# Optimization experiments

Hardware: AMD Instinct MI355X
Metric: run time of the kernel (lower is better)

The kernel has to match this reference:

```python
import jax, jax.numpy as jnp
import numpy as np

TOPK = 4
TEMP = 1.0
BN_EPS = 1e-5


def setup_inputs() -> dict:
    key = jax.random.key(0)
    ks = jax.random.split(key, 5)
    B, H, W = 8, 256, 256
    return {
        "img": jax.random.uniform(ks[0], (B, 3, H, W), dtype=jnp.float32),
        "feat": jax.random.normal(ks[1], (B, 64, H, W), dtype=jnp.float32),
        "w_bneck": jax.random.normal(ks[2], (16, 64), dtype=jnp.float32) * 0.1,
        "b_bneck": jax.random.normal(ks[3], (16,), dtype=jnp.float32) * 0.1,
        "gamma": jnp.ones((16,), dtype=jnp.float32),
        "beta": jnp.zeros((16,), dtype=jnp.float32),
        "w_mask": jax.random.normal(ks[4], (256, 16), dtype=jnp.float32) * 0.1,
        "num_colors": 64,
    }


def reference(img, feat, w_bneck, b_bneck, gamma, beta, w_mask, num_colors):
    B, _, H, W = img.shape
    # bottleneck: 1x1 conv + BatchNorm (training stats) + ReLU
    x = jnp.einsum('bchw,oc->bohw', feat, w_bneck) + b_bneck[None, :, None, None]
    mu = x.mean(axis=(0, 2, 3))
    var = x.var(axis=(0, 2, 3))
    x = (x - mu[None, :, None, None]) * jax.lax.rsqrt(var + BN_EPS)[None, :, None, None]
    x = jax.nn.relu(x * gamma[None, :, None, None] + beta[None, :, None, None])
    # color_mask: bias-free 1x1 conv -> [B, 256, H, W]
    m = jnp.einsum('bchw,oc->bohw', x, w_mask)
    # agg == 'mean': [B, 256//num_colors, num_colors, H, W].mean(1)
    m = m.reshape(B, -1, num_colors, H, W).mean(axis=1)  # [B, nc, H, W]
    # per-pixel topk over color channel + softmax + scatter mask
    k = min(TOPK, num_colors)
    m_l = jnp.transpose(m, (0, 2, 3, 1))          # [B, H, W, nc]
    vals, idx = jax.lax.top_k(m_l, k)             # [B, H, W, k]
    sm = jax.nn.softmax(vals / TEMP, axis=-1)
    bi = jnp.arange(B)[:, None, None, None]
    hi = jnp.arange(H)[None, :, None, None]
    wi = jnp.arange(W)[None, None, :, None]
    m_scat = jnp.zeros_like(m_l).at[bi, hi, wi, idx].set(sm)
    m = jnp.transpose(m_scat, (0, 3, 1, 2))       # [B, nc, H, W]
    # weighted color palette: [B, 3, nc, 1, 1]
    num = jnp.einsum('bchw,bnhw->bcn', img, m)
    den = m.sum(axis=(2, 3))                      # [B, nc]
    color_palette = (num / (den[:, None, :] + 1e-8))[:, :, :, None, None]
    # train-mode reconstruction
    transformed_img = jnp.einsum('bnhw,bcn->bchw', m, color_palette[:, :, :, 0, 0])
    return (transformed_img, m, color_palette)
```

## Files before the change

kernel.cpp:

```cpp
#include <hip/hip_runtime.h>

typedef long long ll;

#define PPI   65536
#define NPIX  524288
#define NCH   64
#define NB    16
#define NC    64
#define BN_EPS 1e-5

__global__ __launch_bounds__(256) void k_conv(const float* __restrict__ feat,
                                              const float* __restrict__ wb,
                                              double* __restrict__ gsum,
                                              double* __restrict__ gsq,
                                              float* __restrict__ xout)
{
    const int tid = threadIdx.x;
    const int wave = tid >> 6, lane = tid & 63;
    const int b   = blockIdx.x >> 6;
    const int p0  = ((blockIdx.x & 63) << 10) + (tid << 2);
    const float* fb = feat + (ll)b * NCH * PPI + p0;

    float4 acc[NB];
#pragma unroll
    for (int o = 0; o < NB; ++o) acc[o] = make_float4(0.f, 0.f, 0.f, 0.f);

#pragma unroll 4
    for (int c = 0; c < NCH; ++c) {
        float4 f = *reinterpret_cast<const float4*>(fb + (ll)c * PPI);
#pragma unroll
        for (int o = 0; o < NB; ++o) {
            float wv = wb[o * NCH + c];
            acc[o].x = fmaf(f.x, wv, acc[o].x);
            acc[o].y = fmaf(f.y, wv, acc[o].y);
            acc[o].z = fmaf(f.z, wv, acc[o].z);
            acc[o].w = fmaf(f.w, wv, acc[o].w);
        }
    }

#pragma unroll
    for (int o = 0; o < NB; ++o)
        *reinterpret_cast<float4*>(xout + ((ll)(b * NC + 48 + o)) * PPI + p0) = acc[o];

    __shared__ float red_s[4][NB], red_q[4][NB];
#pragma unroll
    for (int o = 0; o < NB; ++o) {
        float s = (acc[o].x + acc[o].y) + (acc[o].z + acc[o].w);
        float q = fmaf(acc[o].x, acc[o].x, acc[o].y * acc[o].y) +
                  fmaf(acc[o].z, acc[o].z, acc[o].w * acc[o].w);
#pragma unroll
        for (int off = 32; off > 0; off >>= 1) {
            s += __shfl_down(s, off);
            q += __shfl_down(q, off);
        }
        if (lane == 0) { red_s[wave][o] = s; red_q[wave][o] = q; }
    }
    __syncthreads();
    if (tid < NB) {
        atomicAdd(&gsum[tid], (double)red_s[0][tid] + red_s[1][tid] + red_s[2][tid] + red_s[3][tid]);
        atomicAdd(&gsq[tid],  (double)red_q[0][tid] + red_q[1][tid] + red_q[2][tid] + red_q[3][tid]);
    }
}

__global__ __launch_bounds__(256) void k_mask(const float* __restrict__ img,
                                              const float* __restrict__ gamma,
                                              const float* __restrict__ beta,
                                              const float* __restrict__ wm,
                                              const double* __restrict__ gsum,
                                              const double* __restrict__ gsq,
                                              float* __restrict__ den_g,
                                              float* __restrict__ num_g,
                                              float* m_out,
                                              unsigned* __restrict__ idx_out,
                                              float* __restrict__ sm_out)
{
    __shared__ float weff_l[NC][NB];
    __shared__ float den_loc[4][NC];
    __shared__ float num_loc[4][3 * NC];
    __shared__ float scl_l[NB], shf_l[NB];

    const int tid = threadIdx.x;
    const int wave = tid >> 6;
    const int b   = blockIdx.x >> 6;
    const int p0  = ((blockIdx.x & 63) << 10) + (tid << 2);

    for (int i = tid; i < NC * NB; i += 256) {
        int n = i >> 4, o = i & 15;
        weff_l[n][o] = 0.25f * (wm[n * NB + o] + wm[(64 + n) * NB + o] +
                                wm[(128 + n) * NB + o] + wm[(192 + n) * NB + o]);
    }
    for (int i = tid; i < 4 * NC; i += 256) den_loc[i >> 6][i & 63] = 0.f;
    for (int i = tid; i < 4 * 3 * NC; i += 256) num_loc[i / (3 * NC)][i % (3 * NC)] = 0.f;
    if (tid < NB) {
        double mu  = gsum[tid] * (1.0 / NPIX);
        double var = gsq[tid] * (1.0 / NPIX) - mu * mu;
        double sc  = (double)gamma[tid] / sqrt(var + BN_EPS);
        scl_l[tid] = (float)sc;
        shf_l[tid] = (float)((double)beta[tid] - mu * sc);
    }
    __syncthreads();

    float4 xx[NB];
#pragma unroll
    for (int o = 0; o < NB; ++o)
        xx[o] = *reinterpret_cast<const float4*>(m_out + ((ll)(b * NC + 48 + o)) * PPI + p0);
#pragma unroll
    for (int o = 0; o < NB; ++o) {
        float sc = scl_l[o], sh = shf_l[o];
        xx[o].x = fmaxf(0.f, fmaf(xx[o].x, sc, sh));
        xx[o].y = fmaxf(0.f, fmaf(xx[o].y, sc, sh));
        xx[o].z = fmaxf(0.f, fmaf(xx[o].z, sc, sh));
        xx[o].w = fmaxf(0.f, fmaf(xx[o].w, sc, sh));
    }

    float tv[4][4];
    int   ti[4][4];
#pragma unroll
    for (int j = 0; j < 4; ++j)
#pragma unroll
        for (int k = 0; k < 4; ++k) { tv[j][k] = -3.4e38f; ti[j][k] = 0; }

#pragma unroll 2
    for (int n = 0; n < NC; ++n) {
        const float* wr = weff_l[n];
        float4 v = make_float4(0.f, 0.f, 0.f, 0.f);
#pragma unroll
        for (int o = 0; o < NB; ++o) {
            float w = wr[o];
            v.x = fmaf(xx[o].x, w, v.x);
            v.y = fmaf(xx[o].y, w, v.y);
            v.z = fmaf(xx[o].z, w, v.z);
            v.w = fmaf(xx[o].w, w, v.w);
        }
        float vv[4] = {v.x, v.y, v.z, v.w};
#pragma unroll
        for (int j = 0; j < 4; ++j) {
            float x = vv[j];
            bool c0 = x > tv[j][0];
            bool c1 = x > tv[j][1];
            bool c2 = x > tv[j][2];
            bool c3 = x > tv[j][3];
            tv[j][3] = c2 ? tv[j][2] : fmaxf(x, tv[j][3]);
            ti[j][3] = c2 ? ti[j][2] : (c3 ? n : ti[j][3]);
            tv[j][2] = c1 ? tv[j][1] : fmaxf(x, tv[j][2]);
            ti[j][2] = c1 ? ti[j][1] : (c2 ? n : ti[j][2]);
            tv[j][1] = c0 ? tv[j][0] : fmaxf(x, tv[j][1]);
            ti[j][1] = c0 ? ti[j][0] : (c1 ? n : ti[j][1]);
            tv[j][0] = fmaxf(x, tv[j][0]);
            ti[j][0] = c0 ? n : ti[j][0];
        }
    }

    float smx[4][4];
#pragma unroll
    for (int j = 0; j < 4; ++j) {
        float e1 = expf(tv[j][1] - tv[j][0]);
        float e2 = expf(tv[j][2] - tv[j][0]);
        float e3 = expf(tv[j][3] - tv[j][0]);
        float rz = 1.f / (1.f + e1 + e2 + e3);
        smx[j][0] = rz; smx[j][1] = e1 * rz; smx[j][2] = e2 * rz; smx[j][3] = e3 * rz;
    }

#define SEL(j, n) (((ti[j][0] == (n)) ? smx[j][0] : 0.f) + \
                   ((ti[j][1] == (n)) ? smx[j][1] : 0.f) + \
                   ((ti[j][2] == (n)) ? smx[j][2] : 0.f) + \
                   ((ti[j][3] == (n)) ? smx[j][3] : 0.f))
#pragma unroll 1
    for (int n = 0; n < NC; ++n) {
        float4 mv;
        mv.x = SEL(0, n); mv.y = SEL(1, n); mv.z = SEL(2, n); mv.w = SEL(3, n);
        *reinterpret_cast<float4*>(m_out + ((ll)(b * NC + n)) * PPI + p0) = mv;
    }
#undef SEL

    ll gp = (ll)b * PPI + p0;
    uint4 pk;
    pk.x = (unsigned)ti[0][0] | ((unsigned)ti[0][1] << 8) | ((unsigned)ti[0][2] << 16) | ((unsigned)ti[0][3] << 24);
    pk.y = (unsigned)ti[1][0] | ((unsigned)ti[1][1] << 8) | ((unsigned)ti[1][2] << 16) | ((unsigned)ti[1][3] << 24);
    pk.z = (unsigned)ti[2][0] | ((unsigned)ti[2][1] << 8) | ((unsigned)ti[2][2] << 16) | ((unsigned)ti[2][3] << 24);
    pk.w = (unsigned)ti[3][0] | ((unsigned)ti[3][1] << 8) | ((unsigned)ti[3][2] << 16) | ((unsigned)ti[3][3] << 24);
    *reinterpret_cast<uint4*>(idx_out + gp) = pk;
#pragma unroll
    for (int k = 0; k < 4; ++k) {
        float4 sv = make_float4(smx[0][k], smx[1][k], smx[2][k], smx[3][k]);
        *reinterpret_cast<float4*>(sm_out + (ll)k * NPIX + gp) = sv;
    }

    float4 i0 = *reinterpret_cast<const float4*>(img + ((ll)b * 3 + 0) * PPI + p0);
    float4 i1 = *reinterpret_cast<const float4*>(img + ((ll)b * 3 + 1) * PPI + p0);
    float4 i2 = *reinterpret_cast<const float4*>(img + ((ll)b * 3 + 2) * PPI + p0);
    float ir0[4] = {i0.x, i0.y, i0.z, i0.w};
    float ir1[4] = {i1.x, i1.y, i1.z, i1.w};
    float ir2[4] = {i2.x, i2.y, i2.z, i2.w};
#pragma unroll
    for (int j = 0; j < 4; ++j) {
#pragma unroll
        for (int k = 0; k < 4; ++k) {
            float s = smx[j][k];
            int   n = ti[j][k];
            atomicAdd(&den_loc[wave][n], s);
            atomicAdd(&num_loc[wave][0 * NC + n], s * ir0[j]);
            atomicAdd(&num_loc[wave][1 * NC + n], s * ir1[j]);
            atomicAdd(&num_loc[wave][2 * NC + n], s * ir2[j]);
        }
    }
    __syncthreads();
    if (tid < NC)
        atomicAdd(&den_g[b * NC + tid],
                  den_loc[0][tid] + den_loc[1][tid] + den_loc[2][tid] + den_loc[3][tid]);
    if (tid < 3 * NC)
        atomicAdd(&num_g[(ll)b * 3 * NC + tid],
                  num_loc[0][tid] + num_loc[1][tid] + num_loc[2][tid] + num_loc[3][tid]);
}

__global__ __launch_bounds__(256) void k_recon(const unsigned* __restrict__ idx_in,
                                               const float* __restrict__ sm_in,
                                               const float* __restrict__ den_g,
                                               const float* __restrict__ num_g,
                                               float* __restrict__ pal_out,
                                               float* __restrict__ t_out)
{
    __shared__ float pal_l[3][NC];
    __shared__ float rden[NC];
    const int tid = threadIdx.x;
    const int b   = blockIdx.x >> 6;
    const int p0  = ((blockIdx.x & 63) << 10) + (tid << 2);

    if (tid < NC) rden[tid] = 1.f / (den_g[b * NC + tid] + 1e-8f);
    __syncthreads();
    if (tid < 3 * NC) {
        int c = tid >> 6, n = tid & 63;
        pal_l[c][n] = num_g[(ll)b * 3 * NC + tid] * rden[n];
    }
    __syncthreads();
    if ((blockIdx.x & 63) == 0 && tid < 3 * NC)
        pal_out[b * 3 * NC + tid] = pal_l[tid >> 6][tid & 63];

    ll gp = (ll)b * PPI + p0;
    uint4 pk  = *reinterpret_cast<const uint4*>(idx_in + gp);
    float4 s0 = *reinterpret_cast<const float4*>(sm_in + gp);
    float4 s1 = *reinterpret_cast<const float4*>(sm_in + (ll)NPIX + gp);
    float4 s2 = *reinterpret_cast<const float4*>(sm_in + 2ll * NPIX + gp);
    float4 s3 = *reinterpret_cast<const float4*>(sm_in + 3ll * NPIX + gp);
    unsigned pkv[4] = {pk.x, pk.y, pk.z, pk.w};
    float sA[4][4] = {{s0.x, s1.x, s2.x, s3.x}, {s0.y, s1.y, s2.y, s3.y},
                      {s0.z, s1.z, s2.z, s3.z}, {s0.w, s1.w, s2.w, s3.w}};

#pragma unroll
    for (int c = 0; c < 3; ++c) {
        float4 t;
        float* tp = &t.x;
#pragma unroll
        for (int j = 0; j < 4; ++j) {
            unsigned p = pkv[j];
            tp[j] = sA[j][0] * pal_l[c][p & 255] + sA[j][1] * pal_l[c][(p >> 8) & 255] +
                    sA[j][2] * pal_l[c][(p >> 16) & 255] + sA[j][3] * pal_l[c][p >> 24];
        }
        *reinterpret_cast<float4*>(t_out + ((ll)b * 3 + c) * PPI + p0) = t;
    }
}

extern "C" void kernel_launch(void* const* d_in, const int* in_sizes, int n_in,
                              void* d_out, int out_size, void* d_ws, size_t ws_size,
                              hipStream_t stream)
{
    const float* img   = (const float*)d_in[0];
    const float* feat  = (const float*)d_in[1];
    const float* wb    = (const float*)d_in[2];
    const float* gamma = (const float*)d_in[4];
    const float* beta  = (const float*)d_in[5];
    const float* wm    = (const float*)d_in[6];

    char* ws = (char*)d_ws;
    double*   gsum  = (double*)(ws + 0);
    double*   gsq   = (double*)(ws + 128);
    float*    den_g = (float*)(ws + 256);
    float*    num_g = (float*)(ws + 2304);
    unsigned* idx4  = (unsigned*)(ws + 8448);
    float*    smarr = (float*)(ws + 8448 + 4ll * NPIX);

    float* t_out   = (float*)d_out;
    float* m_out   = t_out + 3ll * NPIX;
    float* pal_out = m_out + 64ll * NPIX;

    hipMemsetAsync(ws, 0, 8448, stream);

    k_conv <<<NPIX / 1024, 256, 0, stream>>>(feat, wb, gsum, gsq, m_out);
    k_mask <<<NPIX / 1024, 256, 0, stream>>>(img, gamma, beta, wm, gsum, gsq,
                                             den_g, num_g, m_out, idx4, smarr);
    k_recon<<<NPIX / 1024, 256, 0, stream>>>(idx4, smarr, den_g, num_g, pal_out, t_out);
}
```

Before: 356.0 us.

## Process one pixel per thread and raise occupancy across all three kernels

Each thread now handles one pixel instead of four, and the grid is four times larger in all three kernels. Launch bounds now request 8 blocks per CU. The aim is to cut per-thread register pressure so more waves are resident to hide memory latency on this bandwidth-bound pipeline. The cost is scalar 4-byte loads and stores instead of float4 vector accesses, four times as many global atomics for BN stats and palette sums, and more per-block setup work such as the weff shared-memory build.

Result: slower. 375.8 us (+5.6%).

```diff
diff --git a/kernel.cpp b/kernel.cpp
--- a/kernel.cpp
+++ b/kernel.cpp
@@ -9,45 +9,40 @@
 #define NC    64
 #define BN_EPS 1e-5
 
-__global__ __launch_bounds__(256) void k_conv(const float* __restrict__ feat,
-                                              const float* __restrict__ wb,
-                                              double* __restrict__ gsum,
-                                              double* __restrict__ gsq,
-                                              float* __restrict__ xout)
-{
-    const int tid = threadIdx.x;
+
+__global__ __launch_bounds__(256, 8) void k_conv(const float* __restrict__ feat,
+                                                 const float* __restrict__ wb,
+                                                 double* __restrict__ gsum,
+                                                 double* __restrict__ gsq,
+                                                 float* __restrict__ xout)
+{
+    const int tid  = threadIdx.x;
     const int wave = tid >> 6, lane = tid & 63;
-    const int b   = blockIdx.x >> 6;
-    const int p0  = ((blockIdx.x & 63) << 10) + (tid << 2);
-    const float* fb = feat + (ll)b * NCH * PPI + p0;
-
-    float4 acc[NB];
-#pragma unroll
-    for (int o = 0; o < NB; ++o) acc[o] = make_float4(0.f, 0.f, 0.f, 0.f);
+    const int b    = blockIdx.x >> 8;
+    const int p    = ((blockIdx.x & 255) << 8) + tid;
+    const float* fb = feat + (ll)b * NCH * PPI + p;
+
+    float acc[NB];
+#pragma unroll
+    for (int o = 0; o < NB; ++o) acc[o] = 0.f;
 
 #pragma unroll 4
     for (int c = 0; c < NCH; ++c) {
-        float4 f = *reinterpret_cast<const float4*>(fb + (ll)c * PPI);
-#pragma unroll
-        for (int o = 0; o < NB; ++o) {
-            float wv = wb[o * NCH + c];
-            acc[o].x = fmaf(f.x, wv, acc[o].x);
-            acc[o].y = fmaf(f.y, wv, acc[o].y);
-            acc[o].z = fmaf(f.z, wv, acc[o].z);
-            acc[o].w = fmaf(f.w, wv, acc[o].w);
-        }
+        float f = fb[(ll)c * PPI];
+#pragma unroll
+        for (int o = 0; o < NB; ++o)
+            acc[o] = fmaf(f, wb[o * NCH + c], acc[o]);
     }
 
 #pragma unroll
     for (int o = 0; o < NB; ++o)
-        *reinterpret_cast<float4*>(xout + ((ll)(b * NC + 48 + o)) * PPI + p0) = acc[o];
+        xout[((ll)(b * NC + 48 + o)) * PPI + p] = acc[o];
 
     __shared__ float red_s[4][NB], red_q[4][NB];
 #pragma unroll
     for (int o = 0; o < NB; ++o) {
-        float s = (acc[o].x + acc[o].y) + (acc[o].z + acc[o].w);
-        float q = fmaf(acc[o].x, acc[o].x, acc[o].y * acc[o].y) +
-                  fmaf(acc[o].z, acc[o].z, acc[o].w * acc[o].w);
+        float s = acc[o];
+        float q = acc[o] * acc[o];
 #pragma unroll
         for (int off = 32; off > 0; off >>= 1) {
             s += __shfl_down(s, off);
@@ -62,27 +57,27 @@
     }
 }
 
-__global__ __launch_bounds__(256) void k_mask(const float* __restrict__ img,
-                                              const float* __restrict__ gamma,
-                                              const float* __restrict__ beta,
-                                              const float* __restrict__ wm,
-                                              const double* __restrict__ gsum,
-                                              const double* __restrict__ gsq,
-                                              float* __restrict__ den_g,
-                                              float* __restrict__ num_g,
-                                              float* m_out,
-                                              unsigned* __restrict__ idx_out,
-                                              float* __restrict__ sm_out)
+__global__ __launch_bounds__(256, 8) void k_mask(const float* __restrict__ img,
+                                                 const float* __restrict__ gamma,
+                                                 const float* __restrict__ beta,
+                                                 const float* __restrict__ wm,
+                                                 const double* __restrict__ gsum,
+                                                 const double* __restrict__ gsq,
+                                                 float* __restrict__ den_g,
+                                                 float* __restrict__ num_g,
+                                                 float* m_out,
+                                                 unsigned* __restrict__ idx_out,
+                                                 float* __restrict__ sm_out)
 {
     __shared__ float weff_l[NC][NB];
     __shared__ float den_loc[4][NC];
     __shared__ float num_loc[4][3 * NC];
     __shared__ float scl_l[NB], shf_l[NB];
 
-    const int tid = threadIdx.x;
+    const int tid  = threadIdx.x;
     const int wave = tid >> 6;
-    const int b   = blockIdx.x >> 6;
-    const int p0  = ((blockIdx.x & 63) << 10) + (tid << 2);
+    const int b    = blockIdx.x >> 8;
+    const int p    = ((blockIdx.x & 255) << 8) + tid;
 
     for (int i = tid; i < NC * NB; i += 256) {
         int n = i >> 4, o = i & 15;
@@ -100,109 +95,69 @@
     }
     __syncthreads();
 
-    float4 xx[NB];
+    float xx[NB];
 #pragma unroll
     for (int o = 0; o < NB; ++o)
-        xx[o] = *reinterpret_cast<const float4*>(m_out + ((ll)(b * NC + 48 + o)) * PPI + p0);
-#pragma unroll
-    for (int o = 0; o < NB; ++o) {
-        float sc = scl_l[o], sh = shf_l[o];
-        xx[o].x = fmaxf(0.f, fmaf(xx[o].x, sc, sh));
-        xx[o].y = fmaxf(0.f, fmaf(xx[o].y, sc, sh));
-        xx[o].z = fmaxf(0.f, fmaf(xx[o].z, sc, sh));
-        xx[o].w = fmaxf(0.f, fmaf(xx[o].w, sc, sh));
-    }
-
-    float tv[4][4];
-    int   ti[4][4];
-#pragma unroll
-    for (int j = 0; j < 4; ++j)
-#pragma unroll
-        for (int k = 0; k < 4; ++k) { tv[j][k] = -3.4e38f; ti[j][k] = 0; }
+        xx[o] = m_out[((ll)(b * NC + 48 + o)) * PPI + p];
+#pragma unroll
+    for (int o = 0; o < NB; ++o)
+        xx[o] = fmaxf(0.f, fmaf(xx[o], scl_l[o], shf_l[o]));
+
+    float tv[4];
+    int   ti[4];
+#pragma unroll
+    for (int k = 0; k < 4; ++k) { tv[k] = -3.4e38f; ti[k] = 0; }
 
 #pragma unroll 2
     for (int n = 0; n < NC; ++n) {
         const float* wr = weff_l[n];
-        float4 v = make_float4(0.f, 0.f, 0.f, 0.f);
-#pragma unroll
-        for (int o = 0; o < NB; ++o) {
-            float w = wr[o];
-            v.x = fmaf(xx[o].x, w, v.x);
-            v.y = fmaf(xx[o].y, w, v.y);
-            v.z = fmaf(xx[o].z, w, v.z);
-            v.w = fmaf(xx[o].w, w, v.w);
-        }
-        float vv[4] = {v.x, v.y, v.z, v.w};
-#pragma unroll
-        for (int j = 0; j < 4; ++j) {
-            float x = vv[j];
-            bool c0 = x > tv[j][0];
-            bool c1 = x > tv[j][1];
-            bool c2 = x > tv[j][2];
-            bool c3 = x > tv[j][3];
-            tv[j][3] = c2 ? tv[j][2] : fmaxf(x, tv[j][3]);
-            ti[j][3] = c2 ? ti[j][2] : (c3 ? n : ti[j][3]);
-            tv[j][2] = c1 ? tv[j][1] : fmaxf(x, tv[j][2]);
-            ti[j][2] = c1 ? ti[j][1] : (c2 ? n : ti[j][2]);
-            tv[j][1] = c0 ? tv[j][0] : fmaxf(x, tv[j][1]);
-            ti[j][1] = c0 ? ti[j][0] : (c1 ? n : ti[j][1]);
-            tv[j][0] = fmaxf(x, tv[j][0]);
-            ti[j][0] = c0 ? n : ti[j][0];
-        }
-    }
-
-    float smx[4][4];
-#pragma unroll
-    for (int j = 0; j < 4; ++j) {
-        float e1 = expf(tv[j][1] - tv[j][0]);
-        float e2 = expf(tv[j][2] - tv[j][0]);
-        float e3 = expf(tv[j][3] - tv[j][0]);
-        float rz = 1.f / (1.f + e1 + e2 + e3);
-        smx[j][0] = rz; smx[j][1] = e1 * rz; smx[j][2] = e2 * rz; smx[j][3] = e3 * rz;
-    }
-
-#define SEL(j, n) (((ti[j][0] == (n)) ? smx[j][0] : 0.f) + \
-                   ((ti[j][1] == (n)) ? smx[j][1] : 0.f) + \
-                   ((ti[j][2] == (n)) ? smx[j][2] : 0.f) + \
-                   ((ti[j][3] == (n)) ? smx[j][3] : 0.f))
+        float v = 0.f;
+#pragma unroll
+        for (int o = 0; o < NB; ++o) v = fmaf(xx[o], wr[o], v);
+        bool c0 = v > tv[0];
+        bool c1 = v > tv[1];
+        bool c2 = v > tv[2];
+        bool c3 = v > tv[3];
+        tv[3] = c2 ? tv[2] : fmaxf(v, tv[3]);
+        ti[3] = c2 ? ti[2] : (c3 ? n : ti[3]);
+        tv[2] = c1 ? tv[1] : fmaxf(v, tv[2]);
+        ti[2] = c1 ? ti[1] : (c2 ? n : ti[2]);
+        tv[1] = c0 ? tv[0] : fmaxf(v, tv[1]);
+        ti[1] = c0 ? ti[0] : (c1 ? n : ti[1]);
+        tv[0] = fmaxf(v, tv[0]);
+        ti[0] = c0 ? n : ti[0];
+    }
+
+    float e1 = expf(tv[1] - tv[0]);
+    float e2 = expf(tv[2] - tv[0]);
+    float e3 = expf(tv[3] - tv[0]);
+    float rz = 1.f / (1.f + e1 + e2 + e3);
+    float smx[4] = {rz, e1 * rz, e2 * rz, e3 * rz};
+
 #pragma unroll 1
     for (int n = 0; n < NC; ++n) {
-        float4 mv;
-        mv.x = SEL(0, n); mv.y = SEL(1, n); mv.z = SEL(2, n); mv.w = SEL(3, n);
-        *reinterpret_cast<float4*>(m_out + ((ll)(b * NC + n)) * PPI + p0) = mv;
-    }
-#undef SEL
-
-    ll gp = (ll)b * PPI + p0;
-    uint4 pk;
-    pk.x = (unsigned)ti[0][0] | ((unsigned)ti[0][1] << 8) | ((unsigned)ti[0][2] << 16) | ((unsigned)ti[0][3] << 24);
-    pk.y = (unsigned)ti[1][0] | ((unsigned)ti[1][1] << 8) | ((unsigned)ti[1][2] << 16) | ((unsigned)ti[1][3] << 24);
-    pk.z = (unsigned)ti[2][0] | ((unsigned)ti[2][1] << 8) | ((unsigned)ti[2][2] << 16) | ((unsigned)ti[2][3] << 24);
-    pk.w = (unsigned)ti[3][0] | ((unsigned)ti[3][1] << 8) | ((unsigned)ti[3][2] << 16) | ((unsigned)ti[3][3] << 24);
-    *reinterpret_cast<uint4*>(idx_out + gp) = pk;
+        float val = ((ti[0] == n) ? smx[0] : 0.f) + ((ti[1] == n) ? smx[1] : 0.f) +
+                    ((ti[2] == n) ? smx[2] : 0.f) + ((ti[3] == n) ? smx[3] : 0.f);
+        m_out[((ll)(b * NC + n)) * PPI + p] = val;
+    }
+
+    ll gp = (ll)b * PPI + p;
+    idx_out[gp] = (unsigned)ti[0] | ((unsigned)ti[1] << 8) |
+                  ((unsigned)ti[2] << 16) | ((unsigned)ti[3] << 24);
+#pragma unroll
+    for (int k = 0; k < 4; ++k) sm_out[(ll)k * NPIX + gp] = smx[k];
+
+    float i0 = img[((ll)b * 3 + 0) * PPI + p];
+    float i1 = img[((ll)b * 3 + 1) * PPI + p];
+    float i2 = img[((ll)b * 3 + 2) * PPI + p];
 #pragma unroll
     for (int k = 0; k < 4; ++k) {
-        float4 sv = make_float4(smx[0][k], smx[1][k], smx[2][k], smx[3][k]);
-        *reinterpret_cast<float4*>(sm_out + (ll)k * NPIX + gp) = sv;
-    }
-
-    float4 i0 = *reinterpret_cast<const float4*>(img + ((ll)b * 3 + 0) * PPI + p0);
-    float4 i1 = *reinterpret_cast<const float4*>(img + ((ll)b * 3 + 1) * PPI + p0);
-    float4 i2 = *reinterpret_cast<const float4*>(img + ((ll)b * 3 + 2) * PPI + p0);
-    float ir0[4] = {i0.x, i0.y, i0.z, i0.w};
-    float ir1[4] = {i1.x, i1.y, i1.z, i1.w};
-    float ir2[4] = {i2.x, i2.y, i2.z, i2.w};
-#pragma unroll
-    for (int j = 0; j < 4; ++j) {
-#pragma unroll
-        for (int k = 0; k < 4; ++k) {
-            float s = smx[j][k];
-            int   n = ti[j][k];
-            atomicAdd(&den_loc[wave][n], s);
-            atomicAdd(&num_loc[wave][0 * NC + n], s * ir0[j]);
-            atomicAdd(&num_loc[wave][1 * NC + n], s * ir1[j]);
-            atomicAdd(&num_loc[wave][2 * NC + n], s * ir2[j]);
-        }
+        float s = smx[k];
+        int   n = ti[k];
+        atomicAdd(&den_loc[wave][n], s);
+        atomicAdd(&num_loc[wave][0 * NC + n], s * i0);
+        atomicAdd(&num_loc[wave][1 * NC + n], s * i1);
+        atomicAdd(&num_loc[wave][2 * NC + n], s * i2);
     }
     __syncthreads();
     if (tid < NC)
@@ -213,18 +168,18 @@
                   num_loc[0][tid] + num_loc[1][tid] + num_loc[2][tid] + num_loc[3][tid]);
 }
 
-__global__ __launch_bounds__(256) void k_recon(const unsigned* __restrict__ idx_in,
-                                               const float* __restrict__ sm_in,
-                                               const float* __restrict__ den_g,
-                                               const float* __restrict__ num_g,
-                                               float* __restrict__ pal_out,
-                                               float* __restrict__ t_out)
+__global__ __launch_bounds__(256, 8) void k_recon(const unsigned* __restrict__ idx_in,
+                                                  const float* __restrict__ sm_in,
+                                                  const float* __restrict__ den_g,
+                                                  const float* __restrict__ num_g,
+                                                  float* __restrict__ pal_out,
+                                                  float* __restrict__ t_out)
 {
     __shared__ float pal_l[3][NC];
     __shared__ float rden[NC];
     const int tid = threadIdx.x;
-    const int b   = blockIdx.x >> 6;
-    const int p0  = ((blockIdx.x & 63) << 10) + (tid << 2);
+    const int b   = blockIdx.x >> 8;
+    const int p   = ((blockIdx.x & 255) << 8) + tid;
 
     if (tid < NC) rden[tid] = 1.f / (den_g[b * NC + tid] + 1e-8f);
     __syncthreads();
@@ -233,30 +188,22 @@
         pal_l[c][n] = num_g[(ll)b * 3 * NC + tid] * rden[n];
     }
     __syncthreads();
-    if ((blockIdx.x & 63) == 0 && tid < 3 * NC)
+    if ((blockIdx.x & 255) == 0 && tid < 3 * NC)
         pal_out[b * 3 * NC + tid] = pal_l[tid >> 6][tid & 63];
 
-    ll gp = (ll)b * PPI + p0;
-    uint4 pk  = *reinterpret_cast<const uint4*>(idx_in + gp);
-    float4 s0 = *reinterpret_cast<const float4*>(sm_in + gp);
-    float4 s1 = *reinterpret_cast<const float4*>(sm_in + (ll)NPIX + gp);
-    float4 s2 = *reinterpret_cast<const float4*>(sm_in + 2ll * NPIX + gp);
-    float4 s3 = *reinterpret_cast<const float4*>(sm_in + 3ll * NPIX + gp);
-    unsigned pkv[4] = {pk.x, pk.y, pk.z, pk.w};
-    float sA[4][4] = {{s0.x, s1.x, s2.x, s3.x}, {s0.y, s1.y, s2.y, s3.y},
-                      {s0.z, s1.z, s2.z, s3.z}, {s0.w, s1.w, s2.w, s3.w}};
+    ll gp = (ll)b * PPI + p;
+    unsigned pk = idx_in[gp];
+    int t0 = pk & 255, t1 = (pk >> 8) & 255, t2 = (pk >> 16) & 255, t3 = pk >> 24;
+    float s0 = sm_in[gp];
+    float s1 = sm_in[(ll)NPIX + gp];
+    float s2 = sm_in[2ll * NPIX + gp];
+    float s3 = sm_in[3ll * NPIX + gp];
 
 #pragma unroll
     for (int c = 0; c < 3; ++c) {
-        float4 t;
-        float* tp = &t.x;
-#pragma unroll
-        for (int j = 0; j < 4; ++j) {
-            unsigned p = pkv[j];
-            tp[j] = sA[j][0] * pal_l[c][p & 255] + sA[j][1] * pal_l[c][(p >> 8) & 255] +
-                    sA[j][2] * pal_l[c][(p >> 16) & 255] + sA[j][3] * pal_l[c][p >> 24];
-        }
-        *reinterpret_cast<float4*>(t_out + ((ll)b * 3 + c) * PPI + p0) = t;
+        float v = s0 * pal_l[c][t0] + s1 * pal_l[c][t1] +
+                  s2 * pal_l[c][t2] + s3 * pal_l[c][t3];
+        t_out[((ll)b * 3 + c) * PPI + p] = v;
     }
 }
 
@@ -285,8 +232,8 @@
 
     hipMemsetAsync(ws, 0, 8448, stream);
 
-    k_conv <<<NPIX / 1024, 256, 0, stream>>>(feat, wb, gsum, gsq, m_out);
-    k_mask <<<NPIX / 1024, 256, 0, stream>>>(img, gamma, beta, wm, gsum, gsq,
-                                             den_g, num_g, m_out, idx4, smarr);
-    k_recon<<<NPIX / 1024, 256, 0, stream>>>(idx4, smarr, den_g, num_g, pal_out, t_out);
-}
+    k_conv <<<NPIX / 256, 256, 0, stream>>>(feat, wb, gsum, gsq, m_out);
+    k_mask <<<NPIX / 256, 256, 0, stream>>>(img, gamma, beta, wm, gsum, gsq,
+                                            den_g, num_g, m_out, idx4, smarr);
+    k_recon<<<NPIX / 256, 256, 0, stream>>>(idx4, smarr, den_g, num_g, pal_out, t_out);
+}
```

## Halve pixels per thread, double grid, batch channel loads in conv

Applied to the files above, without the earlier changes.

Every kernel now handles 2 pixels per thread with float2 accesses instead of 4 with float4, and the grid doubles to 1024 blocks. Launch bounds ask for 4 blocks per SM. k_conv also groups 8 channel loads before the FMAs to expose more memory-level parallelism. The aim is lower register pressure and more waves in flight on a memory-bound pipeline. The cost is narrower vector accesses, twice as many per-block atomic reductions, and more repeated per-block setup such as the weff and palette tables.

New measurement: 353.9 us. About the same (-0.6%).

```diff
diff --git a/kernel.cpp b/kernel.cpp
--- a/kernel.cpp
+++ b/kernel.cpp
@@ -9,45 +9,50 @@
 #define NC    64
 #define BN_EPS 1e-5
 
-__global__ __launch_bounds__(256) void k_conv(const float* __restrict__ feat,
-                                              const float* __restrict__ wb,
-                                              double* __restrict__ gsum,
-                                              double* __restrict__ gsq,
-                                              float* __restrict__ xout)
-{
-    const int tid = threadIdx.x;
+
+__global__ __launch_bounds__(256, 4) void k_conv(const float* __restrict__ feat,
+                                                 const float* __restrict__ wb,
+                                                 double* __restrict__ gsum,
+                                                 double* __restrict__ gsq,
+                                                 float* __restrict__ xout)
+{
+    const int tid  = threadIdx.x;
     const int wave = tid >> 6, lane = tid & 63;
-    const int b   = blockIdx.x >> 6;
-    const int p0  = ((blockIdx.x & 63) << 10) + (tid << 2);
+    const int b    = blockIdx.x >> 7;
+    const int p0   = ((blockIdx.x & 127) << 9) + (tid << 1);
     const float* fb = feat + (ll)b * NCH * PPI + p0;
 
-    float4 acc[NB];
-#pragma unroll
-    for (int o = 0; o < NB; ++o) acc[o] = make_float4(0.f, 0.f, 0.f, 0.f);
-
-#pragma unroll 4
-    for (int c = 0; c < NCH; ++c) {
-        float4 f = *reinterpret_cast<const float4*>(fb + (ll)c * PPI);
-#pragma unroll
-        for (int o = 0; o < NB; ++o) {
-            float wv = wb[o * NCH + c];
-            acc[o].x = fmaf(f.x, wv, acc[o].x);
-            acc[o].y = fmaf(f.y, wv, acc[o].y);
-            acc[o].z = fmaf(f.z, wv, acc[o].z);
-            acc[o].w = fmaf(f.w, wv, acc[o].w);
+    float2 acc[NB];
+#pragma unroll
+    for (int o = 0; o < NB; ++o) acc[o] = make_float2(0.f, 0.f);
+
+#pragma unroll 2
+    for (int g = 0; g < 8; ++g) {
+        float2 f[8];
+#pragma unroll
+        for (int i = 0; i < 8; ++i)
+            f[i] = *reinterpret_cast<const float2*>(fb + (ll)(g * 8 + i) * PPI);
+#pragma unroll
+        for (int i = 0; i < 8; ++i) {
+            const int c = g * 8 + i;
+#pragma unroll
+            for (int o = 0; o < NB; ++o) {
+                float wv = wb[o * NCH + c];
+                acc[o].x = fmaf(f[i].x, wv, acc[o].x);
+                acc[o].y = fmaf(f[i].y, wv, acc[o].y);
+            }
         }
     }
 
 #pragma unroll
     for (int o = 0; o < NB; ++o)
-        *reinterpret_cast<float4*>(xout + ((ll)(b * NC + 48 + o)) * PPI + p0) = acc[o];
+        *reinterpret_cast<float2*>(xout + ((ll)(b * NC + 48 + o)) * PPI + p0) = acc[o];
 
     __shared__ float red_s[4][NB], red_q[4][NB];
 #pragma unroll
     for (int o = 0; o < NB; ++o) {
-        float s = (acc[o].x + acc[o].y) + (acc[o].z + acc[o].w);
-        float q = fmaf(acc[o].x, acc[o].x, acc[o].y * acc[o].y) +
-                  fmaf(acc[o].z, acc[o].z, acc[o].w * acc[o].w);
+        float s = acc[o].x + acc[o].y;
+        float q = fmaf(acc[o].x, acc[o].x, acc[o].y * acc[o].y);
 #pragma unroll
         for (int off = 32; off > 0; off >>= 1) {
             s += __shfl_down(s, off);
@@ -62,27 +67,27 @@
     }
 }
 
-__global__ __launch_bounds__(256) void k_mask(const float* __restrict__ img,
-                                              const float* __restrict__ gamma,
-                                              const float* __restrict__ beta,
-                                              const float* __restrict__ wm,
-                                              const double* __restrict__ gsum,
-                                              const double* __restrict__ gsq,
-                                              float* __restrict__ den_g,
-                                              float* __restrict__ num_g,
-                                              float* m_out,
-                                              unsigned* __restrict__ idx_out,
-                                              float* __restrict__ sm_out)
+__global__ __launch_bounds__(256, 4) void k_mask(const float* __restrict__ img,
+                                                 const float* __restrict__ gamma,
+                                                 const float* __restrict__ beta,
+                                                 const float* __restrict__ wm,
+                                                 const double* __restrict__ gsum,
+                                                 const double* __restrict__ gsq,
+                                                 float* __restrict__ den_g,
+                                                 float* __restrict__ num_g,
+                                                 float* m_out,
+                                                 unsigned* __restrict__ idx_out,
+                                                 float* __restrict__ sm_out)
 {
     __shared__ float weff_l[NC][NB];
     __shared__ float den_loc[4][NC];
     __shared__ float num_loc[4][3 * NC];
     __shared__ float scl_l[NB], shf_l[NB];
 
-    const int tid = threadIdx.x;
+    const int tid  = threadIdx.x;
     const int wave = tid >> 6;
-    const int b   = blockIdx.x >> 6;
-    const int p0  = ((blockIdx.x & 63) << 10) + (tid << 2);
+    const int b    = blockIdx.x >> 7;
+    const int p0   = ((blockIdx.x & 127) << 9) + (tid << 1);
 
     for (int i = tid; i < NC * NB; i += 256) {
         int n = i >> 4, o = i & 15;
@@ -100,41 +105,37 @@
     }
     __syncthreads();
 
-    float4 xx[NB];
+    float2 xx[NB];
 #pragma unroll
     for (int o = 0; o < NB; ++o)
-        xx[o] = *reinterpret_cast<const float4*>(m_out + ((ll)(b * NC + 48 + o)) * PPI + p0);
+        xx[o] = *reinterpret_cast<const float2*>(m_out + ((ll)(b * NC + 48 + o)) * PPI + p0);
 #pragma unroll
     for (int o = 0; o < NB; ++o) {
         float sc = scl_l[o], sh = shf_l[o];
         xx[o].x = fmaxf(0.f, fmaf(xx[o].x, sc, sh));
         xx[o].y = fmaxf(0.f, fmaf(xx[o].y, sc, sh));
-        xx[o].z = fmaxf(0.f, fmaf(xx[o].z, sc, sh));
-        xx[o].w = fmaxf(0.f, fmaf(xx[o].w, sc, sh));
-    }
-
-    float tv[4][4];
-    int   ti[4][4];
-#pragma unroll
-    for (int j = 0; j < 4; ++j)
+    }
+
+    float tv[2][4];
+    int   ti[2][4];
+#pragma unroll
+    for (int j = 0; j < 2; ++j)
 #pragma unroll
         for (int k = 0; k < 4; ++k) { tv[j][k] = -3.4e38f; ti[j][k] = 0; }
 
 #pragma unroll 2
     for (int n = 0; n < NC; ++n) {
         const float* wr = weff_l[n];
-        float4 v = make_float4(0.f, 0.f, 0.f, 0.f);
+        float2 v = make_float2(0.f, 0.f);
 #pragma unroll
         for (int o = 0; o < NB; ++o) {
             float w = wr[o];
             v.x = fmaf(xx[o].x, w, v.x);
             v.y = fmaf(xx[o].y, w, v.y);
-            v.z = fmaf(xx[o].z, w, v.z);
-            v.w = fmaf(xx[o].w, w, v.w);
-        }
-        float vv[4] = {v.x, v.y, v.z, v.w};
-#pragma unroll
-        for (int j = 0; j < 4; ++j) {
+        }
+        float vv[2] = {v.x, v.y};
+#pragma unroll
+        for (int j = 0; j < 2; ++j) {
             float x = vv[j];
             bool c0 = x > tv[j][0];
             bool c1 = x > tv[j][1];
@@ -151,9 +152,9 @@
         }
     }
 
-    float smx[4][4];
-#pragma unroll
-    for (int j = 0; j < 4; ++j) {
+    float smx[2][4];
+#pragma unroll
+    for (int j = 0; j < 2; ++j) {
         float e1 = expf(tv[j][1] - tv[j][0]);
         float e2 = expf(tv[j][2] - tv[j][0]);
         float e3 = expf(tv[j][3] - tv[j][0]);
@@ -167,33 +168,31 @@
                    ((ti[j][3] == (n)) ? smx[j][3] : 0.f))
 #pragma unroll 1
     for (int n = 0; n < NC; ++n) {
-        float4 mv;
-        mv.x = SEL(0, n); mv.y = SEL(1, n); mv.z = SEL(2, n); mv.w = SEL(3, n);
-        *reinterpret_cast<float4*>(m_out + ((ll)(b * NC + n)) * PPI + p0) = mv;
+        float2 mv;
+        mv.x = SEL(0, n); mv.y = SEL(1, n);
+        *reinterpret_cast<float2*>(m_out + ((ll)(b * NC + n)) * PPI + p0) = mv;
     }
 #undef SEL
 
     ll gp = (ll)b * PPI + p0;
-    uint4 pk;
+    uint2 pk;
     pk.x = (unsigned)ti[0][0] | ((unsigned)ti[0][1] << 8) | ((unsigned)ti[0][2] << 16) | ((unsigned)ti[0][3] << 24);
     pk.y = (unsigned)ti[1][0] | ((unsigned)ti[1][1] << 8) | ((unsigned)ti[1][2] << 16) | ((unsigned)ti[1][3] << 24);
-    pk.z = (unsigned)ti[2][0] | ((unsigned)ti[2][1] << 8) | ((unsigned)ti[2][2] << 16) | ((unsigned)ti[2][3] << 24);
-    pk.w = (unsigned)ti[3][0] | ((unsigned)ti[3][1] << 8) | ((unsigned)ti[3][2] << 16) | ((unsigned)ti[3][3] << 24);
-    *reinterpret_cast<uint4*>(idx_out + gp) = pk;
+    *reinterpret_cast<uint2*>(idx_out + gp) = pk;
 #pragma unroll
     for (int k = 0; k < 4; ++k) {
-        float4 sv = make_float4(smx[0][k], smx[1][k], smx[2][k], smx[3][k]);
-        *reinterpret_cast<float4*>(sm_out + (ll)k * NPIX + gp) = sv;
-    }
-
-    float4 i0 = *reinterpret_cast<const float4*>(img + ((ll)b * 3 + 0) * PPI + p0);
-    float4 i1 = *reinterpret_cast<const float4*>(img + ((ll)b * 3 + 1) * PPI + p0);
-    float4 i2 = *reinterpret_cast<const float4*>(img + ((ll)b * 3 + 2) * PPI + p0);
-    float ir0[4] = {i0.x, i0.y, i0.z, i0.w};
-    float ir1[4] = {i1.x, i1.y, i1.z, i1.w};
-    float ir2[4] = {i2.x, i2.y, i2.z, i2.w};
-#pragma unroll
-    for (int j = 0; j < 4; ++j) {
+        float2 sv = make_float2(smx[0][k], smx[1][k]);
+        *reinterpret_cast<float2*>(sm_out + (ll)k * NPIX + gp) = sv;
+    }
+
+    float2 i0 = *reinterpret_cast<const float2*>(img + ((ll)b * 3 + 0) * PPI + p0);
+    float2 i1 = *reinterpret_cast<const float2*>(img + ((ll)b * 3 + 1) * PPI + p0);
+    float2 i2 = *reinterpret_cast<const float2*>(img + ((ll)b * 3 + 2) * PPI + p0);
+    float ir0[2] = {i0.x, i0.y};
+    float ir1[2] = {i1.x, i1.y};
+    float ir2[2] = {i2.x, i2.y};
+#pragma unroll
+    for (int j = 0; j < 2; ++j) {
 #pragma unroll
         for (int k = 0; k < 4; ++k) {
             float s = smx[j][k];
@@ -213,18 +212,18 @@
                   num_loc[0][tid] + num_loc[1][tid] + num_loc[2][tid] + num_loc[3][tid]);
 }
 
-__global__ __launch_bounds__(256) void k_recon(const unsigned* __restrict__ idx_in,
-                                               const float* __restrict__ sm_in,
-                                               const float* __restrict__ den_g,
-                                               const float* __restrict__ num_g,
-                                               float* __restrict__ pal_out,
-                                               float* __restrict__ t_out)
+__global__ __launch_bounds__(256, 4) void k_recon(const unsigned* __restrict__ idx_in,
+                                                  const float* __restrict__ sm_in,
+                                                  const float* __restrict__ den_g,
+                                                  const float* __restrict__ num_g,
+                                                  float* __restrict__ pal_out,
+                                                  float* __restrict__ t_out)
 {
     __shared__ float pal_l[3][NC];
     __shared__ float rden[NC];
     const int tid = threadIdx.x;
-    const int b   = blockIdx.x >> 6;
-    const int p0  = ((blockIdx.x & 63) << 10) + (tid << 2);
+    const int b   = blockIdx.x >> 7;
+    const int p0  = ((blockIdx.x & 127) << 9) + (tid << 1);
 
     if (tid < NC) rden[tid] = 1.f / (den_g[b * NC + tid] + 1e-8f);
     __syncthreads();
@@ -233,30 +232,29 @@
         pal_l[c][n] = num_g[(ll)b * 3 * NC + tid] * rden[n];
     }
     __syncthreads();
-    if ((blockIdx.x & 63) == 0 && tid < 3 * NC)
+    if ((blockIdx.x & 127) == 0 && tid < 3 * NC)
         pal_out[b * 3 * NC + tid] = pal_l[tid >> 6][tid & 63];
 
     ll gp = (ll)b * PPI + p0;
-    uint4 pk  = *reinterpret_cast<const uint4*>(idx_in + gp);
-    float4 s0 = *reinterpret_cast<const float4*>(sm_in + gp);
-    float4 s1 = *reinterpret_cast<const float4*>(sm_in + (ll)NPIX + gp);
-    float4 s2 = *reinterpret_cast<const float4*>(sm_in + 2ll * NPIX + gp);
-    float4 s3 = *reinterpret_cast<const float4*>(sm_in + 3ll * NPIX + gp);
-    unsigned pkv[4] = {pk.x, pk.y, pk.z, pk.w};
-    float sA[4][4] = {{s0.x, s1.x, s2.x, s3.x}, {s0.y, s1.y, s2.y, s3.y},
-                      {s0.z, s1.z, s2.z, s3.z}, {s0.w, s1.w, s2.w, s3.w}};
+    uint2  pk = *reinterpret_cast<const uint2*>(idx_in + gp);
+    float2 s0 = *reinterpret_cast<const float2*>(sm_in + gp);
+    float2 s1 = *reinterpret_cast<const float2*>(sm_in + (ll)NPIX + gp);
+    float2 s2 = *reinterpret_cast<const float2*>(sm_in + 2ll * NPIX + gp);
+    float2 s3 = *reinterpret_cast<const float2*>(sm_in + 3ll * NPIX + gp);
+    unsigned pkv[2] = {pk.x, pk.y};
+    float sA[2][4] = {{s0.x, s1.x, s2.x, s3.x}, {s0.y, s1.y, s2.y, s3.y}};
 
 #pragma unroll
     for (int c = 0; c < 3; ++c) {
-        float4 t;
-        float* tp = &t.x;
-#pragma unroll
-        for (int j = 0; j < 4; ++j) {
-            unsigned p = pkv[j];
-            tp[j] = sA[j][0] * pal_l[c][p & 255] + sA[j][1] * pal_l[c][(p >> 8) & 255] +
-                    sA[j][2] * pal_l[c][(p >> 16) & 255] + sA[j][3] * pal_l[c][p >> 24];
-        }
-        *reinterpret_cast<float4*>(t_out + ((ll)b * 3 + c) * PPI + p0) = t;
+        float2 t;
+#pragma unroll
+        for (int j = 0; j < 2; ++j) {
+            unsigned pv = pkv[j];
+            float v = sA[j][0] * pal_l[c][pv & 255] + sA[j][1] * pal_l[c][(pv >> 8) & 255] +
+                      sA[j][2] * pal_l[c][(pv >> 16) & 255] + sA[j][3] * pal_l[c][pv >> 24];
+            (j == 0 ? t.x : t.y) = v;
+        }
+        *reinterpret_cast<float2*>(t_out + ((ll)b * 3 + c) * PPI + p0) = t;
     }
 }
 
@@ -285,8 +283,8 @@
 
     hipMemsetAsync(ws, 0, 8448, stream);
 
-    k_conv <<<NPIX / 1024, 256, 0, stream>>>(feat, wb, gsum, gsq, m_out);
-    k_mask <<<NPIX / 1024, 256, 0, stream>>>(img, gamma, beta, wm, gsum, gsq,
-                                             den_g, num_g, m_out, idx4, smarr);
-    k_recon<<<NPIX / 1024, 256, 0, stream>>>(idx4, smarr, den_g, num_g, pal_out, t_out);
-}
+    k_conv <<<NPIX / 512, 256, 0, stream>>>(feat, wb, gsum, gsq, m_out);
+    k_mask <<<NPIX / 512, 256, 0, stream>>>(img, gamma, beta, wm, gsum, gsq,
+                                            den_g, num_g, m_out, idx4, smarr);
+    k_recon<<<NPIX / 512, 256, 0, stream>>>(idx4, smarr, den_g, num_g, pal_out, t_out);
+}
```
